# Optimization experiments

Hardware: AMD Instinct MI355X
Metric: run time of the kernel (lower is better)

## Reference

```python
import jax, jax.numpy as jnp
import numpy as np

H_OUT, W_OUT = 473, 473  # original image size the logits are upsampled to
BN_EPS = 1e-5


def _conv(x, w, pad):
    return jax.lax.conv_general_dilated(
        x, w, window_strides=(1, 1), padding=[(pad, pad), (pad, pad)],
        dimension_numbers=('NCHW', 'OIHW', 'NCHW'))


def _bn(x, g, b):
    # BatchNorm2d in training mode: batch statistics over (N, H, W)
    m = jnp.mean(x, axis=(0, 2, 3), keepdims=True)
    v = jnp.var(x, axis=(0, 2, 3), keepdims=True)
    return (x - m) * jax.lax.rsqrt(v + BN_EPS) * g.reshape(1, -1, 1, 1) + b.reshape(1, -1, 1, 1)


def setup_inputs() -> dict:
    key = jax.random.key(0)
    ks = jax.random.split(key, 8)
    B, C, Hf, Wf, NC = 2, 256, 60, 60, 2
    return {
        'V_a': jax.random.normal(ks[0], (B, C, Hf, Wf), jnp.float32),
        'V_b': jax.random.normal(ks[1], (B, C, Hf, Wf), jnp.float32),
        'D_a': jax.random.normal(ks[2], (B, C, Hf, Wf), jnp.float32),
        'W_e': jax.random.normal(ks[3], (C, C), jnp.float32) * 0.02,
        'gate_w': jax.random.normal(ks[4], (1, C, 1, 1), jnp.float32) * 0.01,
        'conv1_w': jax.random.normal(ks[5], (C, 3 * C, 3, 3), jnp.float32) * 0.01,
        'conv2_w': jax.random.normal(ks[6], (C, 2 * C, 3, 3), jnp.float32) * 0.01,
        'bn1_g': jnp.ones((C,), jnp.float32),
        'bn1_b': jnp.zeros((C,), jnp.float32),
        'bn2_g': jnp.ones((C,), jnp.float32),
        'bn2_b': jnp.zeros((C,), jnp.float32),
        'cls1_w': jax.random.normal(ks[7], (NC, C, 1, 1), jnp.float32) * 0.01,
        'cls1_b': jnp.zeros((NC,), jnp.float32),
        'cls2_w': jax.random.normal(jax.random.fold_in(key, 9), (NC, C, 1, 1), jnp.float32) * 0.01,
        'cls2_b': jnp.zeros((NC,), jnp.float32),
    }


def reference(V_a, V_b, D_a, W_e, gate_w, conv1_w, conv2_w,
              bn1_g, bn1_b, bn2_g, bn2_b, cls1_w, cls1_b, cls2_w, cls2_b):
    B, C, Hf, Wf = V_a.shape
    N = Hf * Wf
    V_a_flat = V_a.reshape(B, C, N)
    V_b_flat = V_b.reshape(B, C, N)

    # linear_e on transposed A features, then affinity S = (A^T W^T) B
    weighted = jnp.einsum('bcn,dc->bnd', V_a_flat, W_e)        # [B, N, C]
    S = jnp.einsum('bnd,bdm->bnm', weighted, V_b_flat)         # [B, N, N]

    S_row = jax.nn.softmax(S, axis=1)                          # softmax over dim 1
    S_colT = jax.nn.softmax(jnp.swapaxes(S, 1, 2), axis=1)     # softmax of S^T over dim 1

    Z_b = jnp.einsum('bcn,bnm->bcm', V_a_flat, S_row)          # attended for view b
    Z_a = jnp.einsum('bcn,bnm->bcm', V_b_flat, S_colT)         # attended for view a

    att1 = Z_a.reshape(B, C, Hf, Wf)
    att2 = Z_b.reshape(B, C, Hf, Wf)

    # 1x1 sigmoid gates
    att1 = att1 * jax.nn.sigmoid(_conv(att1, gate_w, 0))
    att2 = att2 * jax.nn.sigmoid(_conv(att2, gate_w, 0))

    # conc1: branch-1 concatenates gated attention, RGB feat, and depth feat
    x1 = jnp.concatenate([att1, V_a, D_a], axis=1)             # [B, 3C, Hf, Wf]
    x2 = jnp.concatenate([att2, V_b], axis=1)                  # [B, 2C, Hf, Wf]

    x1 = jax.nn.relu(_bn(_conv(x1, conv1_w, 1), bn1_g, bn1_b))
    x2 = jax.nn.relu(_bn(_conv(x2, conv2_w, 1), bn2_g, bn2_b))

    x1 = _conv(x1, cls1_w, 0) + cls1_b.reshape(1, -1, 1, 1)
    x2 = _conv(x2, cls2_w, 0) + cls2_b.reshape(1, -1, 1, 1)

    NC = cls1_w.shape[0]
    x1 = jax.image.resize(x1, (B, NC, H_OUT, W_OUT), 'linear')
    x2 = jax.image.resize(x2, (B, NC, H_OUT, W_OUT), 'linear')
    return jax.nn.sigmoid(x1), jax.nn.sigmoid(x2)
```

## Files before the change

### kernel.cpp

```cpp
#include <hip/hip_runtime.h>

#define BB 2
#define CC 256
#define NN 3600
#define NCH 2
#define HO 473
#define WO 473
#define NP 3648
#define NR 3712
#define NTI 29
#define ZKS 6

typedef unsigned short u16;
typedef __attribute__((ext_vector_type(8))) short short8;
typedef __attribute__((ext_vector_type(4))) float f32x4;

static __device__ __forceinline__ u16 f2bf(float f) {
    unsigned u = __float_as_uint(f);
    unsigned r = (u + 0x7FFF + ((u >> 16) & 1)) >> 16;
    return (u16)r;
}
static __device__ __forceinline__ u16 f2h(float f) {
    _Float16 h = (_Float16)f;
    return __builtin_bit_cast(unsigned short, h);
}
static __device__ __forceinline__ float h2f(u16 u) {
    _Float16 h = __builtin_bit_cast(_Float16, u);
    return (float)h;
}

static __device__ __forceinline__ void glds16(const u16* g, u16* l) {
    __builtin_amdgcn_global_load_lds(
        (const __attribute__((address_space(1))) void*)g,
        (__attribute__((address_space(3))) void*)l, 16, 0, 0);
}


__global__ __launch_bounds__(256)
void gemm_we(const u16* __restrict__ vat, const u16* __restrict__ web,
             u16* __restrict__ wgtb)
{
    __shared__ u16 As[128 * 64];
    __shared__ u16 Bs[128 * 64];
    const u16* A = vat + (long)blockIdx.z * NR * CC;
    u16* Cp = wgtb + (long)blockIdx.z * NR * CC;

    const int t = threadIdx.x;
    const int w = t >> 6, lane = t & 63;
    const int mh = (w >> 1) * 64, nh = (w & 1) * 64;
    const int lm = lane & 15, quad = lane >> 4;
    const int m0 = blockIdx.y * 128, n0 = blockIdx.x * 128;
    const int wb = t & 192;

    f32x4 acc[4][4] = {};

    for (int k0 = 0; k0 < CC; k0 += 64) {
#pragma unroll
        for (int i = 0; i < 4; ++i) {
            int idx = i * 256 + t;
            int row = idx >> 3;
            int sc8 = ((idx ^ row) & 7) * 8;
            glds16(A + (long)(m0 + row) * CC + k0 + sc8, &As[(i * 256 + wb) * 8]);
            glds16(web + (long)(n0 + row) * CC + k0 + sc8, &Bs[(i * 256 + wb) * 8]);
        }
        __syncthreads();
#pragma unroll
        for (int s = 0; s < 2; ++s) {
            short8 a[4], b[4];
#pragma unroll
            for (int i = 0; i < 4; ++i)
                a[i] = *(const short8*)(&As[(mh + i * 16 + lm) * 64 + ((s * 4 + quad) ^ (lm & 7)) * 8]);
#pragma unroll
            for (int j = 0; j < 4; ++j)
                b[j] = *(const short8*)(&Bs[(nh + j * 16 + lm) * 64 + ((s * 4 + quad) ^ (lm & 7)) * 8]);
#pragma unroll
            for (int i = 0; i < 4; ++i)
#pragma unroll
                for (int j = 0; j < 4; ++j)
                    acc[i][j] = __builtin_amdgcn_mfma_f32_16x16x32_bf16(a[i], b[j], acc[i][j], 0, 0, 0);
        }
        __syncthreads();
    }
#pragma unroll
    for (int i = 0; i < 4; ++i)
#pragma unroll
        for (int r = 0; r < 4; ++r) {
            int row = m0 + mh + i * 16 + quad * 4 + r;
            if (row < NN)
#pragma unroll
                for (int j = 0; j < 4; ++j) {
                    int col = n0 + nh + j * 16 + lm;
                    if (col < CC) Cp[(long)row * CC + col] = f2bf(acc[i][j][r]);
                }
        }
}

__global__ __launch_bounds__(256)
void gemm_s_stats(const u16* __restrict__ A, const u16* __restrict__ B,
                  u16* __restrict__ Sh, u16* __restrict__ STh,
                  float* __restrict__ prowm, float* __restrict__ prows,
                  float* __restrict__ pcolm, float* __restrict__ pcols)
{
    __shared__ u16 smem[17408];
    u16* As = smem;
    u16* Bs = smem + 8192;

    const int t = threadIdx.x;
    const int w = t >> 6, lane = t & 63;
    const int mh = (w >> 1) * 64, nh = (w & 1) * 64;
    const int lm = lane & 15, quad = lane >> 4;
    const int m0 = blockIdx.y * 128, n0 = blockIdx.x * 128;
    const int wb = t & 192;

    f32x4 acc[4][4] = {};

    for (int k0 = 0; k0 < CC; k0 += 64) {
#pragma unroll
        for (int i = 0; i < 4; ++i) {
            int idx = i * 256 + t;
            int row = idx >> 3;
            int sc8 = ((idx ^ row) & 7) * 8;
            glds16(A + (long)(m0 + row) * CC + k0 + sc8, &As[(i * 256 + wb) * 8]);
            glds16(B + (long)(n0 + row) * CC + k0 + sc8, &Bs[(i * 256 + wb) * 8]);
        }
        __syncthreads();
#pragma unroll
        for (int s = 0; s < 2; ++s) {
            short8 a[4], b[4];
#pragma unroll
            for (int i = 0; i < 4; ++i)
                a[i] = *(const short8*)(&As[(mh + i * 16 + lm) * 64 + ((s * 4 + quad) ^ (lm & 7)) * 8]);
#pragma unroll
            for (int j = 0; j < 4; ++j)
                b[j] = *(const short8*)(&Bs[(nh + j * 16 + lm) * 64 + ((s * 4 + quad) ^ (lm & 7)) * 8]);
#pragma unroll
            for (int i = 0; i < 4; ++i)
#pragma unroll
                for (int j = 0; j < 4; ++j)
                    acc[i][j] = __builtin_amdgcn_mfma_f32_16x16x32_bf16(a[i], b[j], acc[i][j], 0, 0, 0);
        }
        __syncthreads();
    }

#pragma unroll
    for (int i = 0; i < 4; ++i)
#pragma unroll
        for (int r = 0; r < 4; ++r) {
            int row = m0 + mh + i * 16 + quad * 4 + r;
            if (row < NN)
#pragma unroll
                for (int j = 0; j < 4; ++j) {
                    int col = n0 + nh + j * 16 + lm;
                    if (col < NN) Sh[(long)row * NP + col] = f2h(acc[i][j][r]);
                }
        }

    bool cval[4];
#pragma unroll
    for (int j = 0; j < 4; ++j) cval[j] = (n0 + nh + j * 16 + lm) < NN;

    float* sm = (float*)smem;
    float* rowm = sm;
    float* rows_ = sm + 256;
    float* colm = sm + 512;
    float* cols_ = sm + 768;
    __syncthreads();

#pragma unroll
    for (int i = 0; i < 4; ++i)
#pragma unroll
        for (int r = 0; r < 4; ++r) {
            float m = -3.0e38f;
#pragma unroll
            for (int j = 0; j < 4; ++j) if (cval[j]) m = fmaxf(m, acc[i][j][r]);
            m = fmaxf(m, __shfl_xor(m, 1, 64));
            m = fmaxf(m, __shfl_xor(m, 2, 64));
            m = fmaxf(m, __shfl_xor(m, 4, 64));
            m = fmaxf(m, __shfl_xor(m, 8, 64));
            float s = 0.f;
#pragma unroll
            for (int j = 0; j < 4; ++j) if (cval[j]) s += __expf(acc[i][j][r] - m);
            s += __shfl_xor(s, 1, 64);
            s += __shfl_xor(s, 2, 64);
            s += __shfl_xor(s, 4, 64);
            s += __shfl_xor(s, 8, 64);
            if (lm == 0) {
                int rr = mh + i * 16 + quad * 4 + r;
                rowm[(w & 1) * 128 + rr] = m;
                rows_[(w & 1) * 128 + rr] = s;
            }
        }

#pragma unroll
    for (int j = 0; j < 4; ++j) {
        float m = -3.0e38f;
#pragma unroll
        for (int i = 0; i < 4; ++i)
#pragma unroll
            for (int r = 0; r < 4; ++r)
                if (m0 + mh + i * 16 + quad * 4 + r < NN) m = fmaxf(m, acc[i][j][r]);
        m = fmaxf(m, __shfl_xor(m, 16, 64));
        m = fmaxf(m, __shfl_xor(m, 32, 64));
        float s = 0.f;
#pragma unroll
        for (int i = 0; i < 4; ++i)
#pragma unroll
            for (int r = 0; r < 4; ++r)
                if (m0 + mh + i * 16 + quad * 4 + r < NN) s += __expf(acc[i][j][r] - m);
        s += __shfl_xor(s, 16, 64);
        s += __shfl_xor(s, 32, 64);
        if (quad == 0) {
            int ccl = nh + j * 16 + lm;
            colm[(w >> 1) * 128 + ccl] = m;
            cols_[(w >> 1) * 128 + ccl] = s;
        }
    }
    __syncthreads();

    if (t < 128) {
        float m1 = rowm[t], m2 = rowm[128 + t];
        float M = fmaxf(m1, m2);
        float s = rows_[t] * __expf(m1 - M) + rows_[128 + t] * __expf(m2 - M);
        if (m0 + t < NN) {
            prowm[(long)blockIdx.x * NR + m0 + t] = M;
            prows[(long)blockIdx.x * NR + m0 + t] = s;
        }
    } else {
        int c = t - 128;
        float m1 = colm[c], m2 = colm[128 + c];
        float M = fmaxf(m1, m2);
        float s = cols_[c] * __expf(m1 - M) + cols_[128 + c] * __expf(m2 - M);
        if (n0 + c < NN) {
            pcolm[(long)blockIdx.y * NR + n0 + c] = M;
            pcols[(long)blockIdx.y * NR + n0 + c] = s;
        }
    }

    __syncthreads();
    u16* tr = smem;
#pragma unroll
    for (int i = 0; i < 4; ++i)
#pragma unroll
        for (int j = 0; j < 4; ++j)
#pragma unroll
            for (int r = 0; r < 4; ++r)
                tr[(nh + j * 16 + lm) * 136 + (mh + i * 16 + quad * 4 + r)] = f2h(acc[i][j][r]);
    __syncthreads();
    {
        int row = t >> 1, hf = t & 1;
        int mg = n0 + row;
        if (mg < NN) {
#pragma unroll
            for (int q = 0; q < 8; ++q) {
                int cb = m0 + hf * 64 + q * 8;
                if (cb < NN)
                    *(uint4*)(&STh[(long)mg * NP + cb]) =
                        *(const uint4*)(&tr[row * 136 + hf * 64 + q * 8]);
            }
        }
    }
}

__global__ __launch_bounds__(256)
void stats_combine(const float* __restrict__ prowm, const float* __restrict__ prows,
                   const float* __restrict__ pcolm, const float* __restrict__ pcols,
                   float* __restrict__ rmx, float* __restrict__ rsm,
                   float* __restrict__ cmx, float* __restrict__ csm)
{
    int i = blockIdx.x * 256 + threadIdx.x;
    if (i >= NN) return;
    const float* pm = blockIdx.y ? pcolm : prowm;
    const float* ps = blockIdx.y ? pcols : prows;
    float m = -3.0e38f, s = 0.f;
#pragma unroll 4
    for (int tI = 0; tI < NTI; ++tI) {
        float m2 = pm[(long)tI * NR + i], s2 = ps[(long)tI * NR + i];
        float M = fmaxf(m, m2);
        s = s * __expf(m - M) + s2 * __expf(m2 - M);
        m = M;
    }
    if (blockIdx.y) { cmx[i] = m; csm[i] = s; }
    else            { rmx[i] = m; rsm[i] = s; }
}

__global__ __launch_bounds__(256)
void p_build(u16* __restrict__ Sh, u16* __restrict__ STh,
             const float* __restrict__ rmx, const float* __restrict__ rsm,
             const float* __restrict__ cmx, const float* __restrict__ csm)
{
    int r = blockIdx.x;
    u16* M = blockIdx.y ? STh : Sh;
    const float* mx = blockIdx.y ? cmx : rmx;
    const float* sm = blockIdx.y ? csm : rsm;
    float mv = mx[r];
    float inv = 1.f / sm[r];
    u16* row = M + (long)r * NP;
    int t = threadIdx.x;
    for (int c0 = t * 8; c0 < NP; c0 += 2048) {
        uint4 hv = *(const uint4*)(row + c0);
        const u16* hp = (const u16*)&hv;
        u16 o[8];
#pragma unroll
        for (int e = 0; e < 8; ++e) {
            int c = c0 + e;
            o[e] = (c < NN) ? f2bf(__expf(h2f(hp[e]) - mv) * inv) : (u16)0;
        }
        *(uint4*)(row + c0) = *(const uint4*)o;
    }
}

__global__ __launch_bounds__(256, 4)
void gemm_z_128(const u16* __restrict__ vab_b, const u16* __restrict__ vbb_b,
                const u16* __restrict__ PT, const u16* __restrict__ P,
                float* __restrict__ Zb_b, float* __restrict__ Za_b)
{
    __shared__ u16 As[128 * 64];
    __shared__ u16 Bs[128 * 64];

    const int t = threadIdx.x;
    const int w = t >> 6, lane = t & 63;
    const int mh = (w >> 1) * 64, nh = (w & 1) * 64;
    const int lm = lane & 15, quad = lane >> 4;
    const int n0 = blockIdx.x * 128;
    const int ks = blockIdx.y;
    const int zz = blockIdx.z;
    const int branch = zz & 1;
    const int m0 = (zz >> 1) * 128;
    const u16* A = branch ? vbb_b : vab_b;
    const u16* B = branch ? P : PT;
    float* Cp = branch ? Za_b : Zb_b;
    const int wb = t & 192;

    const int base = 57 / ZKS, rem = 57 % ZKS;
    const int it0 = ks * base + (ks < rem ? ks : rem);
    const int itn = base + (ks < rem ? 1 : 0);

    f32x4 acc[4][4] = {};

    for (int it = it0; it < it0 + itn; ++it) {
        const int k0 = it * 64;
#pragma unroll
        for (int i = 0; i < 4; ++i) {
            int idx = i * 256 + t;
            int row = idx >> 3;
            int sc8 = ((idx ^ row) & 7) * 8;
            glds16(A + (long)(m0 + row) * NP + k0 + sc8, &As[(i * 256 + wb) * 8]);
            glds16(B + (long)(n0 + row) * NP + k0 + sc8, &Bs[(i * 256 + wb) * 8]);
        }
        __syncthreads();
#pragma unroll
        for (int s = 0; s < 2; ++s) {
            short8 a[4], b[4];
#pragma unroll
            for (int i = 0; i < 4; ++i)
                a[i] = *(const short8*)(&As[(mh + i * 16 + lm) * 64 + ((s * 4 + quad) ^ (lm & 7)) * 8]);
#pragma unroll
            for (int j = 0; j < 4; ++j)
                b[j] = *(const short8*)(&Bs[(nh + j * 16 + lm) * 64 + ((s * 4 + quad) ^ (lm & 7)) * 8]);
#pragma unroll
            for (int i = 0; i < 4; ++i)
#pragma unroll
                for (int j = 0; j < 4; ++j)
                    acc[i][j] = __builtin_amdgcn_mfma_f32_16x16x32_bf16(a[i], b[j], acc[i][j], 0, 0, 0);
        }
        __syncthreads();
    }

#pragma unroll
    for (int i = 0; i < 4; ++i)
#pragma unroll
        for (int r = 0; r < 4; ++r) {
            int row = m0 + mh + i * 16 + quad * 4 + r;
#pragma unroll
            for (int j = 0; j < 4; ++j) {
                int col = n0 + nh + j * 16 + lm;
                if (col < NN)
                    atomicAdd(&Cp[(long)row * NN + col], acc[i][j][r]);
            }
        }
}

__global__ __launch_bounds__(256, 4)
void conv_both(const u16* __restrict__ W1, const u16* __restrict__ W2,
               const u16* __restrict__ gzaT, const u16* __restrict__ vat,
               const u16* __restrict__ daT, const u16* __restrict__ gzbT,
               const u16* __restrict__ vbt, const u16* __restrict__ zbuf,
               float* __restrict__ y1, float* __restrict__ y2)
{
    __shared__ u16 As[128 * 64];
    __shared__ u16 Bs[128 * 64];

    const int t = threadIdx.x;
    const int w = t >> 6, lane = t & 63;
    const int mh = (w >> 1) * 64, nh = (w & 1) * 64;
    const int lm = lane & 15, quad = lane >> 4;
    const int wb = t & 192;

    const long L = blockIdx.x + (long)NTI * (blockIdx.y + (long)ZKS * blockIdx.z);
    const int combo = (int)(L & 7);
    const long rest = L >> 3;
    const int ks = (int)(rest % ZKS);
    const int px = (int)(rest / ZKS);
    const int which = combo >> 2;
    const int b = (combo >> 1) & 1;
    const int m0 = (combo & 1) * 128;
    const int n0 = px * 128;

    const int CIN = which ? 512 : 768;
    const int KT = 9 * CIN;
    const u16* W = which ? W2 : W1;
    const u16* P0 = which ? gzbT : gzaT;
    const u16* P1 = which ? vbt : vat;
    const u16* P2 = which ? vbt : daT;
    float* Y = which ? y2 : y1;
    const long pstride = (long)NR * CC;

    const int per = (KT / 64) / ZKS;
    const int it0 = ks * per;

    int pv[4], hv[4], wv[4], sc8v[4];
#pragma unroll
    for (int i = 0; i < 4; ++i) {
        int idx = i * 256 + t;
        int row = idx >> 3;
        sc8v[i] = ((idx ^ row) & 7) * 8;
        pv[i] = n0 + row;
        hv[i] = pv[i] / 60;
        wv[i] = pv[i] - hv[i] * 60;
    }

    f32x4 acc[4][4] = {};

    for (int it = it0; it < it0 + per; ++it) {
        const int k0 = it * 64;
        int tap = k0 / CIN;
        int kloc = k0 - tap * CIN;
        int plane = kloc >> 8, cip = kloc & 255;
        int dh = tap / 3 - 1, dw = tap - (tap / 3) * 3 - 1;
        int off = dh * 60 + dw;
        const u16* src = (plane == 0) ? P0 : ((plane == 1) ? P1 : P2);
        src += (long)b * pstride + cip;

#pragma unroll
        for (int i = 0; i < 4; ++i) {
            int idx = i * 256 + t;
            int row = idx >> 3;
            glds16(W + (long)(m0 + row) * KT + k0 + sc8v[i], &As[(i * 256 + wb) * 8]);
            bool ok = pv[i] < NN && (unsigned)(hv[i] + dh) < 60u && (unsigned)(wv[i] + dw) < 60u;
            const u16* gs = ok ? src + (long)(pv[i] + off) * CC + sc8v[i] : zbuf;
            glds16(gs, &Bs[(i * 256 + wb) * 8]);
        }
        __syncthreads();
#pragma unroll
        for (int s = 0; s < 2; ++s) {
            short8 a[4], bfr[4];
#pragma unroll
            for (int i = 0; i < 4; ++i)
                a[i] = *(const short8*)(&As[(mh + i * 16 + lm) * 64 + ((s * 4 + quad) ^ (lm & 7)) * 8]);
#pragma unroll
            for (int j = 0; j < 4; ++j)
                bfr[j] = *(const short8*)(&Bs[(nh + j * 16 + lm) * 64 + ((s * 4 + quad) ^ (lm & 7)) * 8]);
#pragma unroll
            for (int i = 0; i < 4; ++i)
#pragma unroll
                for (int j = 0; j < 4; ++j)
                    acc[i][j] = __builtin_amdgcn_mfma_f32_16x16x32_bf16(a[i], bfr[j], acc[i][j], 0, 0, 0);
        }
        __syncthreads();
    }

    float* out = Y + (long)b * CC * NN;
#pragma unroll
    for (int i = 0; i < 4; ++i)
#pragma unroll
        for (int r = 0; r < 4; ++r) {
            int row = m0 + mh + i * 16 + quad * 4 + r;
#pragma unroll
            for (int j = 0; j < 4; ++j) {
                int col = n0 + nh + j * 16 + lm;
                if (col < NN)
                    atomicAdd(&out[(long)row * NN + col], acc[i][j][r]);
            }
        }
}

__global__ __launch_bounds__(256)
void cvt_we(const float* __restrict__ W, u16* __restrict__ O)
{
    int i = blockIdx.x * 256 + threadIdx.x;
    if (i < CC * CC) O[i] = f2bf(W[i]);
}

__global__ __launch_bounds__(256)
void transpose_cvt(const float* __restrict__ V, u16* __restrict__ VT,
                   u16* __restrict__ Vpad)
{
    __shared__ float tile[64][65];
    int b = blockIdx.z, c0 = blockIdx.y * 64, n0 = blockIdx.x * 64;
    int t = threadIdx.x;
#pragma unroll
    for (int e = 0; e < 16; ++e) {
        int f = e * 256 + t; int i = f >> 6, j = f & 63;
        int n = n0 + j;
        float v = 0.f;
        if (n < NN) v = V[((long)b * CC + c0 + i) * NN + n];
        tile[i][j] = v;
        if (Vpad) Vpad[((long)b * CC + c0 + i) * NP + n] = f2bf(v);
    }
    __syncthreads();
#pragma unroll
    for (int e = 0; e < 16; ++e) {
        int f = e * 256 + t; int i = f >> 6, j = f & 63;
        int n = n0 + i;
        if (n < NN) VT[((long)b * NR + n) * CC + c0 + j] = f2bf(tile[j][i]);
    }
}

__global__ __launch_bounds__(256)
void transpose_gate(const float* __restrict__ Z, const float* __restrict__ sg,
                    u16* __restrict__ ZT)
{
    __shared__ float tile[64][65];
    int b = blockIdx.z, c0 = blockIdx.y * 64, n0 = blockIdx.x * 64;
    int t = threadIdx.x;
#pragma unroll
    for (int e = 0; e < 16; ++e) {
        int f = e * 256 + t; int i = f >> 6, j = f & 63;
        int n = n0 + j;
        float v = 0.f;
        if (n < NN) v = Z[((long)b * CC + c0 + i) * NN + n];
        tile[i][j] = v;
    }
    __syncthreads();
#pragma unroll
    for (int e = 0; e < 16; ++e) {
        int f = e * 256 + t; int i = f >> 6, j = f & 63;
        int n = n0 + i;
        if (n < NN)
            ZT[((long)b * NR + n) * CC + c0 + j] = f2bf(tile[j][i] * sg[b * NN + n]);
    }
}

template<int CIN>
__global__ __launch_bounds__(256)
void cvt_convw(const float* __restrict__ W, u16* __restrict__ O)
{
    const int KT = 9 * CIN;
    long idx = (long)blockIdx.x * 256 + threadIdx.x;
    if (idx >= (long)CC * KT) return;
    int co = (int)(idx / KT);
    int r = (int)(idx % KT);
    int tap = r / CIN, ci = r % CIN;
    O[idx] = f2bf(W[((long)co * CIN + ci) * 9 + tap]);
}

__global__ __launch_bounds__(256)
void gate_sig(const float* __restrict__ Z, const float* __restrict__ gw,
              float* __restrict__ sg)
{
    int t = threadIdx.x;
    int px = t & 63, ck = t >> 6;
    int b = blockIdx.y;
    int p = blockIdx.x * 64 + px;
    const float* Zp = Z + (long)b * CC * NN;
    float g = 0.f;
    if (p < NN) {
        for (int c = ck * 64; c < ck * 64 + 64; ++c) g += gw[c] * Zp[(long)c * NN + p];
    }
    __shared__ float red[256];
    red[t] = g;
    __syncthreads();
    if (t < 64) {
        int pp = blockIdx.x * 64 + t;
        if (pp < NN) {
            float tot = red[t] + red[t + 64] + red[t + 128] + red[t + 192];
            sg[b * NN + pp] = 1.f / (1.f + __expf(-tot));
        }
    }
}

__global__ __launch_bounds__(256)
void bn_stats_kernel(const float* __restrict__ Y, const float* __restrict__ g,
                     const float* __restrict__ beta, float* __restrict__ scale,
                     float* __restrict__ shift)
{
    int c = blockIdx.x, t = threadIdx.x;
    float s = 0.f, sq = 0.f;
    for (int b = 0; b < BB; ++b) {
        const float* p = Y + (long)b * CC * NN + (long)c * NN;
        for (int i = t; i < NN; i += 256) { float v = p[i]; s += v; sq += v * v; }
    }
    __shared__ float ls[256], lq[256];
    ls[t] = s; lq[t] = sq;
    __syncthreads();
    for (int off = 128; off > 0; off >>= 1) {
        if (t < off) { ls[t] += ls[t + off]; lq[t] += lq[t + off]; }
        __syncthreads();
    }
    if (t == 0) {
        const float inv = 1.f / (float)(BB * NN);
        float mean = ls[0] * inv;
        float var = fmaxf(lq[0] * inv - mean * mean, 0.f);
        float sc = g[c] * rsqrtf(var + 1e-5f);
        scale[c] = sc;
        shift[c] = beta[c] - mean * sc;
    }
}

__global__ __launch_bounds__(256)
void cls_kernel(const float* __restrict__ Y, const float* __restrict__ scale,
                const float* __restrict__ shift, const float* __restrict__ cw,
                const float* __restrict__ cb, float* __restrict__ O)
{
    int t = threadIdx.x;
    int px = t & 63, ck = t >> 6;
    int b = blockIdx.y;
    int p = blockIdx.x * 64 + px;
    const float* Yb = Y + (long)b * CC * NN;
    float a0 = 0.f, a1 = 0.f;
    if (p < NN) {
        for (int c = ck * 64; c < ck * 64 + 64; ++c) {
            float v = Yb[(long)c * NN + p] * scale[c] + shift[c];
            v = fmaxf(v, 0.f);
            a0 += cw[c] * v;
            a1 += cw[CC + c] * v;
        }
    }
    __shared__ float r0[256], r1[256];
    r0[t] = a0; r1[t] = a1;
    __syncthreads();
    if (t < 64) {
        int pp = blockIdx.x * 64 + t;
        if (pp < NN) {
            float s0 = r0[t] + r0[t + 64] + r0[t + 128] + r0[t + 192];
            float s1 = r1[t] + r1[t + 64] + r1[t + 128] + r1[t + 192];
            O[(long)b * NCH * NN + pp] = s0 + cb[0];
            O[(long)b * NCH * NN + NN + pp] = s1 + cb[1];
        }
    }
}

__global__ __launch_bounds__(256)
void resize_sig_kernel(const float* __restrict__ I1, const float* __restrict__ I2,
                       float* __restrict__ O)
{
    const long HALF = (long)BB * NCH * HO * WO;
    long gid = (long)blockIdx.x * 256 + threadIdx.x;
    if (gid >= HALF) return;
    int half = blockIdx.y;
    const float* I = half ? I2 : I1;
    float* Op = O + half * HALF;

    int j = (int)(gid % WO);
    long r = gid / WO;
    int i = (int)(r % HO);
    int pc = (int)(r / HO);
    const float* ip = I + (long)pc * NN;

    const float SCL = 60.0f / 473.0f;
    float fy = (i + 0.5f) * SCL - 0.5f;
    float fx = (j + 0.5f) * SCL - 0.5f;
    int y0 = (int)floorf(fy);
    int x0 = (int)floorf(fx);
    float ty = fy - (float)y0;
    float tx = fx - (float)x0;
    int y0c = max(y0, 0), y1c = min(y0 + 1, 59);
    int x0c = max(x0, 0), x1c = min(x0 + 1, 59);
    float va = ip[y0c * 60 + x0c], vb = ip[y0c * 60 + x1c];
    float vc = ip[y1c * 60 + x0c], vd = ip[y1c * 60 + x1c];
    float v = (1.f - ty) * ((1.f - tx) * va + tx * vb) + ty * ((1.f - tx) * vc + tx * vd);
    Op[gid] = 1.f / (1.f + __expf(-v));
}

extern "C" void kernel_launch(void* const* d_in, const int* in_sizes, int n_in,
                              void* d_out, int out_size, void* d_ws, size_t ws_size,
                              hipStream_t stream)
{
    const float* V_a    = (const float*)d_in[0];
    const float* V_b    = (const float*)d_in[1];
    const float* D_a    = (const float*)d_in[2];
    const float* W_e    = (const float*)d_in[3];
    const float* gate_w = (const float*)d_in[4];
    const float* conv1_w = (const float*)d_in[5];
    const float* conv2_w = (const float*)d_in[6];
    const float* bn1_g = (const float*)d_in[7];
    const float* bn1_b = (const float*)d_in[8];
    const float* bn2_g = (const float*)d_in[9];
    const float* bn2_b = (const float*)d_in[10];
    const float* cls1_w = (const float*)d_in[11];
    const float* cls1_b = (const float*)d_in[12];
    const float* cls2_w = (const float*)d_in[13];
    const float* cls2_b = (const float*)d_in[14];
    float* out = (float*)d_out;

    size_t off = 0;
    char* wsb = (char*)d_ws;
    auto carve = [&](size_t bytes) -> char* {
        char* p = wsb + off; off += (bytes + 255) & ~(size_t)255; return p;
    };

    u16* Sh    = (u16*)carve((size_t)NR * NP * 2);
    u16* STh   = (u16*)carve((size_t)NR * NP * 2);
    u16* vab   = (u16*)carve((size_t)BB * CC * NP * 2);
    u16* vbb   = (u16*)carve((size_t)BB * CC * NP * 2);
    u16* vat   = (u16*)carve((size_t)BB * NR * CC * 2);
    u16* vbt   = (u16*)carve((size_t)BB * NR * CC * 2);
    u16* daT   = (u16*)carve((size_t)BB * NR * CC * 2);
    u16* gzaT  = (u16*)carve((size_t)BB * NR * CC * 2);
    u16* gzbT  = (u16*)carve((size_t)BB * NR * CC * 2);
    u16* wgtb  = (u16*)carve((size_t)BB * NR * CC * 2);
    u16* zbuf  = (u16*)carve(256);
    u16* web   = (u16*)carve((size_t)CC * CC * 2);
    u16* wt1   = (u16*)carve((size_t)CC * 9 * 768 * 2);
    u16* wt2   = (u16*)carve((size_t)CC * 9 * 512 * 2);
    float* Za  = (float*)carve((size_t)BB * CC * NN * 4);
    float* Zb  = (float*)carve((size_t)BB * CC * NN * 4);
    float* y1  = (float*)carve((size_t)BB * CC * NN * 4);
    float* y2  = (float*)carve((size_t)BB * CC * NN * 4);
    float* rmx = (float*)carve((size_t)BB * NN * 4);
    float* rsm = (float*)carve((size_t)BB * NN * 4);
    float* cmx = (float*)carve((size_t)BB * NN * 4);
    float* csm = (float*)carve((size_t)BB * NN * 4);
    float* sga = (float*)carve((size_t)BB * NN * 4);
    float* sgb = (float*)carve((size_t)BB * NN * 4);
    float* prm = (float*)carve((size_t)NTI * NR * 4);
    float* prs = (float*)carve((size_t)NTI * NR * 4);
    float* pcm = (float*)carve((size_t)NTI * NR * 4);
    float* pcs = (float*)carve((size_t)NTI * NR * 4);
    float* c1o = (float*)carve((size_t)BB * NCH * NN * 4);
    float* c2o = (float*)carve((size_t)BB * NCH * NN * 4);

    dim3 blk(256);

    hipMemsetAsync(Za, 0, (size_t)4 * BB * CC * NN * 4, stream);
    hipMemsetAsync(vat, 0, (size_t)6 * ((size_t)BB * NR * CC * 2) + 256, stream);

    cvt_we<<<256, blk, 0, stream>>>(W_e, web);
    transpose_cvt<<<dim3(57, 4, BB), blk, 0, stream>>>(V_a, vat, vab);
    transpose_cvt<<<dim3(57, 4, BB), blk, 0, stream>>>(V_b, vbt, vbb);
    transpose_cvt<<<dim3(57, 4, BB), blk, 0, stream>>>(D_a, daT, nullptr);
    cvt_convw<768><<<(int)(((long)CC * 9 * 768 + 255) / 256), blk, 0, stream>>>(conv1_w, wt1);
    cvt_convw<512><<<(int)(((long)CC * 9 * 512 + 255) / 256), blk, 0, stream>>>(conv2_w, wt2);

    gemm_we<<<dim3(2, NTI, BB), blk, 0, stream>>>(vat, web, wgtb);

    for (int b = 0; b < BB; ++b) {
        const u16* wgtb_b = wgtb + (long)b * NR * CC;
        const u16* vbt_b  = vbt + (long)b * NR * CC;
        const u16* vab_b  = vab + (long)b * CC * NP;
        const u16* vbb_b  = vbb + (long)b * CC * NP;
        float* rmx_b = rmx + b * NN; float* rsm_b = rsm + b * NN;
        float* cmx_b = cmx + b * NN; float* csm_b = csm + b * NN;

        gemm_s_stats<<<dim3(NTI, NTI), blk, 0, stream>>>(
            wgtb_b, vbt_b, Sh, STh, prm, prs, pcm, pcs);
        stats_combine<<<dim3((NN + 255) / 256, 2), blk, 0, stream>>>(
            prm, prs, pcm, pcs, rmx_b, rsm_b, cmx_b, csm_b);
        p_build<<<dim3(NN, 2), blk, 0, stream>>>(Sh, STh, rmx_b, rsm_b, cmx_b, csm_b);
        gemm_z_128<<<dim3(NTI, ZKS, 4), blk, 0, stream>>>(
            vab_b, vbb_b, STh, Sh,
            Zb + (long)b * CC * NN, Za + (long)b * CC * NN);
    }

    gate_sig<<<dim3(57, BB), blk, 0, stream>>>(Za, gate_w, sga);
    gate_sig<<<dim3(57, BB), blk, 0, stream>>>(Zb, gate_w, sgb);
    transpose_gate<<<dim3(57, 4, BB), blk, 0, stream>>>(Za, sga, gzaT);
    transpose_gate<<<dim3(57, 4, BB), blk, 0, stream>>>(Zb, sgb, gzbT);

    conv_both<<<dim3(NTI, ZKS, 8), blk, 0, stream>>>(
        wt1, wt2, gzaT, vat, daT, gzbT, vbt, zbuf, y1, y2);

    bn_stats_kernel<<<256, blk, 0, stream>>>(y1, bn1_g, bn1_b, rmx, rsm);
    bn_stats_kernel<<<256, blk, 0, stream>>>(y2, bn2_g, bn2_b, cmx, csm);
    cls_kernel<<<dim3(57, BB), blk, 0, stream>>>(y1, rmx, rsm, cls1_w, cls1_b, c1o);
    cls_kernel<<<dim3(57, BB), blk, 0, stream>>>(y2, cmx, csm, cls2_w, cls2_b, c2o);

    resize_sig_kernel<<<dim3((int)(((long)BB * NCH * HO * WO + 255) / 256), 2), blk, 0, stream>>>(c1o, c2o, out);
}
```

Before: 625.1 us.

## Double-buffer LDS tiles with async prefetch in GEMM and conv kernels

Three MFMA GEMM kernels (gemm_we, gemm_z_128, conv_both) now use two LDS buffers. Each iteration issues global-to-LDS loads for the next k-tile before computing the current one, and uses a vmcnt wait plus raw s_barrier in place of the two __syncthreads. The aim is to overlap global memory latency with MFMA work. In exchange, LDS use per block doubles to 64 KB and launch bounds drop from 4 to 2 blocks per CU, so occupancy falls.

```diff
diff --git a/kernel.cpp b/kernel.cpp
--- a/kernel.cpp
+++ b/kernel.cpp
@@ -35,13 +35,17 @@
         (__attribute__((address_space(3))) void*)l, 16, 0, 0);
 }
 
-
-__global__ __launch_bounds__(256)
+template<int N> static __device__ __forceinline__ void vmwait() {
+    asm volatile("s_waitcnt vmcnt(%0)" :: "n"(N) : "memory");
+}
+
+
+__global__ __launch_bounds__(256, 2)
 void gemm_we(const u16* __restrict__ vat, const u16* __restrict__ web,
              u16* __restrict__ wgtb)
 {
-    __shared__ u16 As[128 * 64];
-    __shared__ u16 Bs[128 * 64];
+    __shared__ u16 As[2][128 * 64];
+    __shared__ u16 Bs[2][128 * 64];
     const u16* A = vat + (long)blockIdx.z * NR * CC;
     u16* Cp = wgtb + (long)blockIdx.z * NR * CC;
 
@@ -54,32 +58,47 @@
 
     f32x4 acc[4][4] = {};
 
-    for (int k0 = 0; k0 < CC; k0 += 64) {
+    auto STAGE = [&](int bb, int k0) {
 #pragma unroll
         for (int i = 0; i < 4; ++i) {
             int idx = i * 256 + t;
             int row = idx >> 3;
             int sc8 = ((idx ^ row) & 7) * 8;
-            glds16(A + (long)(m0 + row) * CC + k0 + sc8, &As[(i * 256 + wb) * 8]);
-            glds16(web + (long)(n0 + row) * CC + k0 + sc8, &Bs[(i * 256 + wb) * 8]);
-        }
-        __syncthreads();
+            glds16(A + (long)(m0 + row) * CC + k0 + sc8, &As[bb][(i * 256 + wb) * 8]);
+            glds16(web + (long)(n0 + row) * CC + k0 + sc8, &Bs[bb][(i * 256 + wb) * 8]);
+        }
+    };
+
+    STAGE(0, 0);
+    for (int k0 = 0; k0 < CC; k0 += 64) {
+        const int cur = (k0 >> 6) & 1;
+        if (k0 + 64 < CC) {
+            STAGE(cur ^ 1, k0 + 64);
+            __builtin_amdgcn_sched_barrier(0);
+            vmwait<8>();
+        } else {
+            __builtin_amdgcn_sched_barrier(0);
+            vmwait<0>();
+        }
+        __builtin_amdgcn_s_barrier();
+        __builtin_amdgcn_sched_barrier(0);
 #pragma unroll
         for (int s = 0; s < 2; ++s) {
             short8 a[4], b[4];
 #pragma unroll
             for (int i = 0; i < 4; ++i)
-                a[i] = *(const short8*)(&As[(mh + i * 16 + lm) * 64 + ((s * 4 + quad) ^ (lm & 7)) * 8]);
+                a[i] = *(const short8*)(&As[cur][(mh + i * 16 + lm) * 64 + ((s * 4 + quad) ^ (lm & 7)) * 8]);
 #pragma unroll
             for (int j = 0; j < 4; ++j)
-                b[j] = *(const short8*)(&Bs[(nh + j * 16 + lm) * 64 + ((s * 4 + quad) ^ (lm & 7)) * 8]);
+                b[j] = *(const short8*)(&Bs[cur][(nh + j * 16 + lm) * 64 + ((s * 4 + quad) ^ (lm & 7)) * 8]);
 #pragma unroll
             for (int i = 0; i < 4; ++i)
 #pragma unroll
                 for (int j = 0; j < 4; ++j)
                     acc[i][j] = __builtin_amdgcn_mfma_f32_16x16x32_bf16(a[i], b[j], acc[i][j], 0, 0, 0);
         }
-        __syncthreads();
+        __builtin_amdgcn_sched_barrier(0);
+        __builtin_amdgcn_s_barrier();
     }
 #pragma unroll
     for (int i = 0; i < 4; ++i)
@@ -309,13 +328,13 @@
     }
 }
 
-__global__ __launch_bounds__(256, 4)
+__global__ __launch_bounds__(256, 2)
 void gemm_z_128(const u16* __restrict__ vab_b, const u16* __restrict__ vbb_b,
                 const u16* __restrict__ PT, const u16* __restrict__ P,
                 float* __restrict__ Zb_b, float* __restrict__ Za_b)
 {
-    __shared__ u16 As[128 * 64];
-    __shared__ u16 Bs[128 * 64];
+    __shared__ u16 As[2][128 * 64];
+    __shared__ u16 Bs[2][128 * 64];
 
     const int t = threadIdx.x;
     const int w = t >> 6, lane = t & 63;
@@ -337,33 +356,48 @@
 
     f32x4 acc[4][4] = {};
 
-    for (int it = it0; it < it0 + itn; ++it) {
+    auto STAGE = [&](int bb, int it) {
         const int k0 = it * 64;
 #pragma unroll
         for (int i = 0; i < 4; ++i) {
             int idx = i * 256 + t;
             int row = idx >> 3;
             int sc8 = ((idx ^ row) & 7) * 8;
-            glds16(A + (long)(m0 + row) * NP + k0 + sc8, &As[(i * 256 + wb) * 8]);
-            glds16(B + (long)(n0 + row) * NP + k0 + sc8, &Bs[(i * 256 + wb) * 8]);
-        }
-        __syncthreads();
+            glds16(A + (long)(m0 + row) * NP + k0 + sc8, &As[bb][(i * 256 + wb) * 8]);
+            glds16(B + (long)(n0 + row) * NP + k0 + sc8, &Bs[bb][(i * 256 + wb) * 8]);
+        }
+    };
+
+    STAGE(0, it0);
+    for (int it = it0; it < it0 + itn; ++it) {
+        const int cur = (it - it0) & 1;
+        if (it + 1 < it0 + itn) {
+            STAGE(cur ^ 1, it + 1);
+            __builtin_amdgcn_sched_barrier(0);
+            vmwait<8>();
+        } else {
+            __builtin_amdgcn_sched_barrier(0);
+            vmwait<0>();
+        }
+        __builtin_amdgcn_s_barrier();
+        __builtin_amdgcn_sched_barrier(0);
 #pragma unroll
         for (int s = 0; s < 2; ++s) {
             short8 a[4], b[4];
 #pragma unroll
             for (int i = 0; i < 4; ++i)
-                a[i] = *(const short8*)(&As[(mh + i * 16 + lm) * 64 + ((s * 4 + quad) ^ (lm & 7)) * 8]);
+                a[i] = *(const short8*)(&As[cur][(mh + i * 16 + lm) * 64 + ((s * 4 + quad) ^ (lm & 7)) * 8]);
 #pragma unroll
             for (int j = 0; j < 4; ++j)
-                b[j] = *(const short8*)(&Bs[(nh + j * 16 + lm) * 64 + ((s * 4 + quad) ^ (lm & 7)) * 8]);
+                b[j] = *(const short8*)(&Bs[cur][(nh + j * 16 + lm) * 64 + ((s * 4 + quad) ^ (lm & 7)) * 8]);
 #pragma unroll
             for (int i = 0; i < 4; ++i)
 #pragma unroll
                 for (int j = 0; j < 4; ++j)
                     acc[i][j] = __builtin_amdgcn_mfma_f32_16x16x32_bf16(a[i], b[j], acc[i][j], 0, 0, 0);
         }
-        __syncthreads();
+        __builtin_amdgcn_sched_barrier(0);
+        __builtin_amdgcn_s_barrier();
     }
 
 #pragma unroll
@@ -380,15 +414,15 @@
         }
 }
 
-__global__ __launch_bounds__(256, 4)
+__global__ __launch_bounds__(256, 2)
 void conv_both(const u16* __restrict__ W1, const u16* __restrict__ W2,
                const u16* __restrict__ gzaT, const u16* __restrict__ vat,
                const u16* __restrict__ daT, const u16* __restrict__ gzbT,
                const u16* __restrict__ vbt, const u16* __restrict__ zbuf,
                float* __restrict__ y1, float* __restrict__ y2)
 {
-    __shared__ u16 As[128 * 64];
-    __shared__ u16 Bs[128 * 64];
+    __shared__ u16 As[2][128 * 64];
+    __shared__ u16 Bs[2][128 * 64];
 
     const int t = threadIdx.x;
     const int w = t >> 6, lane = t & 63;
@@ -431,7 +465,7 @@
 
     f32x4 acc[4][4] = {};
 
-    for (int it = it0; it < it0 + per; ++it) {
+    auto STAGE = [&](int bb, int it) {
         const int k0 = it * 64;
         int tap = k0 / CIN;
         int kloc = k0 - tap * CIN;
@@ -440,33 +474,47 @@
         int off = dh * 60 + dw;
         const u16* src = (plane == 0) ? P0 : ((plane == 1) ? P1 : P2);
         src += (long)b * pstride + cip;
-
 #pragma unroll
         for (int i = 0; i < 4; ++i) {
             int idx = i * 256 + t;
             int row = idx >> 3;
-            glds16(W + (long)(m0 + row) * KT + k0 + sc8v[i], &As[(i * 256 + wb) * 8]);
+            glds16(W + (long)(m0 + row) * KT + k0 + sc8v[i], &As[bb][(i * 256 + wb) * 8]);
             bool ok = pv[i] < NN && (unsigned)(hv[i] + dh) < 60u && (unsigned)(wv[i] + dw) < 60u;
             const u16* gs = ok ? src + (long)(pv[i] + off) * CC + sc8v[i] : zbuf;
-            glds16(gs, &Bs[(i * 256 + wb) * 8]);
-        }
-        __syncthreads();
+            glds16(gs, &Bs[bb][(i * 256 + wb) * 8]);
+        }
+    };
+
+    STAGE(0, it0);
+    for (int it = it0; it < it0 + per; ++it) {
+        const int cur = (it - it0) & 1;
+        if (it + 1 < it0 + per) {
+            STAGE(cur ^ 1, it + 1);
+            __builtin_amdgcn_sched_barrier(0);
+            vmwait<8>();
+        } else {
+            __builtin_amdgcn_sched_barrier(0);
+            vmwait<0>();
+        }
+        __builtin_amdgcn_s_barrier();
+        __builtin_amdgcn_sched_barrier(0);
 #pragma unroll
         for (int s = 0; s < 2; ++s) {
             short8 a[4], bfr[4];
 #pragma unroll
             for (int i = 0; i < 4; ++i)
-                a[i] = *(const short8*)(&As[(mh + i * 16 + lm) * 64 + ((s * 4 + quad) ^ (lm & 7)) * 8]);
+                a[i] = *(const short8*)(&As[cur][(mh + i * 16 + lm) * 64 + ((s * 4 + quad) ^ (lm & 7)) * 8]);
 #pragma unroll
             for (int j = 0; j < 4; ++j)
-                bfr[j] = *(const short8*)(&Bs[(nh + j * 16 + lm) * 64 + ((s * 4 + quad) ^ (lm & 7)) * 8]);
+                bfr[j] = *(const short8*)(&Bs[cur][(nh + j * 16 + lm) * 64 + ((s * 4 + quad) ^ (lm & 7)) * 8]);
 #pragma unroll
             for (int i = 0; i < 4; ++i)
 #pragma unroll
                 for (int j = 0; j < 4; ++j)
                     acc[i][j] = __builtin_amdgcn_mfma_f32_16x16x32_bf16(a[i], bfr[j], acc[i][j], 0, 0, 0);
         }
-        __syncthreads();
+        __builtin_amdgcn_sched_barrier(0);
+        __builtin_amdgcn_s_barrier();
     }
 
     float* out = Y + (long)b * CC * NN;
```

Result: slower. 909.7 us (+45.5%).
